# Kernel optimization log

Hardware: AMD Instinct MI355X
Metric: run time of the kernel (lower is better)

The kernel has to match this reference:

```python
import jax, jax.numpy as jnp
import numpy as np

P = 120000   # total pillars across batch
C = 64       # num_input_features
B = 4
NX = 512
NY = 512


def setup_inputs() -> dict:
    key = jax.random.key(0)
    k1, k2, k3, k4 = jax.random.split(key, 4)
    voxel_features = jax.random.normal(k1, (P, C), dtype=jnp.float32)
    b = jax.random.randint(k2, (P, 1), 0, B, dtype=jnp.int32)
    z = jnp.zeros((P, 1), dtype=jnp.int32)
    y = jax.random.randint(k3, (P, 1), 0, NY, dtype=jnp.int32)
    x = jax.random.randint(k4, (P, 1), 0, NX, dtype=jnp.int32)
    coords = jnp.concatenate([b, z, y, x], axis=1)  # [P, 4] = (batch, z, y, x)
    return {"voxel_features": voxel_features, "coords": coords,
            "batch_size": B, "nx": NX, "ny": NY}


def reference(voxel_features, coords, batch_size, nx, ny):
    # Fused scatter: flat index = batch*ny*nx + y*nx + x (single pass, no per-batch loop).
    flat = (coords[:, 0].astype(jnp.int32) * (ny * nx)
            + coords[:, 2].astype(jnp.int32) * nx
            + coords[:, 3].astype(jnp.int32))  # [P]
    canvas = jnp.zeros((batch_size * ny * nx, voxel_features.shape[1]),
                       dtype=voxel_features.dtype)
    canvas = canvas.at[flat].set(voxel_features)          # [B*ny*nx, C]
    canvas = canvas.reshape(batch_size, ny, nx, -1)       # [B, ny, nx, C]
    return canvas.transpose(0, 3, 1, 2)                   # [B, C, ny, nx]
```

## Files before the change

kernel.cpp:

```cpp
#include <hip/hip_runtime.h>
#include <hip/hip_bf16.h>


#define NXC 512
#define NYC 512
#define BC 4
#define CC 64
#define SLOTS_PER_BATCH (NXC * NYC)
#define TOTAL_SLOTS (BC * SLOTS_PER_BATCH)

typedef float vf4 __attribute__((ext_vector_type(4)));

__global__ void build_winner_kernel(const int* __restrict__ coords,
                                    int* __restrict__ winner, int P) {
    int p = blockIdx.x * blockDim.x + threadIdx.x;
    if (p >= P) return;
    int4 c = ((const int4*)coords)[p];
    int flat = c.x * SLOTS_PER_BATCH + c.z * NXC + c.w;
    atomicMax(&winner[flat], p);
}

__global__ __launch_bounds__(256) void scatter_out_kernel(
        const float* __restrict__ vf,
        const int* __restrict__ winner,
        float* __restrict__ out) {
    int blk = blockIdx.x;
    int h   = blk & 1;
    int tq  = ((blk >> 1) << 8) + threadIdx.x;
    int b   = tq >> 16;
    int rem = (tq << 2) & (SLOTS_PER_BATCH - 1);

    int4 w = ((const int4*)winner)[tq];

    float* obase = out + (size_t)b * (CC * SLOTS_PER_BATCH)
                       + (size_t)(h << 5) * SLOTS_PER_BATCH + rem;
    const int coff = h << 3;
    const vf4* v0 = (const vf4*)(vf + (size_t)w.x * CC) + coff;
    const vf4* v1 = (const vf4*)(vf + (size_t)w.y * CC) + coff;
    const vf4* v2 = (const vf4*)(vf + (size_t)w.z * CC) + coff;
    const vf4* v3 = (const vf4*)(vf + (size_t)w.w * CC) + coff;

    const vf4 z4 = (vf4)(0.f);
    #pragma unroll
    for (int j = 0; j < 8; ++j) {
        vf4 a = z4, bb = z4, cc = z4, dd = z4;
        if (w.x >= 0) a  = v0[j];
        if (w.y >= 0) bb = v1[j];
        if (w.z >= 0) cc = v2[j];
        if (w.w >= 0) dd = v3[j];

        vf4* s0 = (vf4*)(obase + (size_t)(4 * j + 0) * SLOTS_PER_BATCH);
        vf4* s1 = (vf4*)(obase + (size_t)(4 * j + 1) * SLOTS_PER_BATCH);
        vf4* s2 = (vf4*)(obase + (size_t)(4 * j + 2) * SLOTS_PER_BATCH);
        vf4* s3 = (vf4*)(obase + (size_t)(4 * j + 3) * SLOTS_PER_BATCH);
        vf4 r0 = {a.x, bb.x, cc.x, dd.x};
        vf4 r1 = {a.y, bb.y, cc.y, dd.y};
        vf4 r2 = {a.z, bb.z, cc.z, dd.z};
        vf4 r3 = {a.w, bb.w, cc.w, dd.w};
        __builtin_nontemporal_store(r0, s0);
        __builtin_nontemporal_store(r1, s1);
        __builtin_nontemporal_store(r2, s2);
        __builtin_nontemporal_store(r3, s3);
    }
}

extern "C" void kernel_launch(void* const* d_in, const int* in_sizes, int n_in,
                              void* d_out, int out_size, void* d_ws, size_t ws_size,
                              hipStream_t stream) {
    const float* vf    = (const float*)d_in[0];
    const int* coords  = (const int*)d_in[1];
    int P = in_sizes[0] / CC;

    int* winner = (int*)d_ws;
    float* out  = (float*)d_out;

    (void)hipMemsetAsync(winner, 0xFF, (size_t)TOTAL_SLOTS * sizeof(int), stream);

    build_winner_kernel<<<(P + 255) / 256, 256, 0, stream>>>(coords, winner, P);

    scatter_out_kernel<<<(TOTAL_SLOTS / 4 / 256) * 2, 256, 0, stream>>>(vf, winner, out);
}
```

Measured before the change: 299.3 us.

## Remap scatter blocks to chunk-by-channel-quad grid with XCD-aware chunk placement

```diff
diff --git a/kernel.cpp b/kernel.cpp
--- a/kernel.cpp
+++ b/kernel.cpp
@@ -8,6 +8,9 @@
 #define CC 64
 #define SLOTS_PER_BATCH (NXC * NYC)
 #define TOTAL_SLOTS (BC * SLOTS_PER_BATCH)
+#define CHUNK_SLOTS 8192
+#define NCHUNK (TOTAL_SLOTS / CHUNK_SLOTS)
+#define NCQ (CC / 4)
 
 typedef float vf4 __attribute__((ext_vector_type(4)));
 
@@ -24,43 +27,41 @@
         const float* __restrict__ vf,
         const int* __restrict__ winner,
         float* __restrict__ out) {
-    int blk = blockIdx.x;
-    int h   = blk & 1;
-    int tq  = ((blk >> 1) << 8) + threadIdx.x;
-    int b   = tq >> 16;
-    int rem = (tq << 2) & (SLOTS_PER_BATCH - 1);
+    int raw = blockIdx.x;
+    int xcd = raw & 7;
+    int i   = raw >> 3;
+    int cq    = i & 15;
+    int chunk = ((i >> 4) << 3) | xcd;
 
-    int4 w = ((const int4*)winner)[tq];
+    int t     = threadIdx.x;
+    int qbase = chunk * (CHUNK_SLOTS / 4);
+    int slot0 = chunk * CHUNK_SLOTS;
+    int b     = slot0 >> 18;
+    int rem0  = slot0 & (SLOTS_PER_BATCH - 1);
 
-    float* obase = out + (size_t)b * (CC * SLOTS_PER_BATCH)
-                       + (size_t)(h << 5) * SLOTS_PER_BATCH + rem;
-    const int coff = h << 3;
-    const vf4* v0 = (const vf4*)(vf + (size_t)w.x * CC) + coff;
-    const vf4* v1 = (const vf4*)(vf + (size_t)w.y * CC) + coff;
-    const vf4* v2 = (const vf4*)(vf + (size_t)w.z * CC) + coff;
-    const vf4* v3 = (const vf4*)(vf + (size_t)w.w * CC) + coff;
+    float* obase = out + ((size_t)b * CC + (size_t)(cq << 2)) * SLOTS_PER_BATCH;
 
     const vf4 z4 = (vf4)(0.f);
     #pragma unroll
-    for (int j = 0; j < 8; ++j) {
+    for (int g = 0; g < 8; ++g) {
+        int q = (g << 8) + t;
+        int4 w = ((const int4*)winner)[qbase + q];
+        int rem = rem0 + (q << 2);
+
         vf4 a = z4, bb = z4, cc = z4, dd = z4;
-        if (w.x >= 0) a  = v0[j];
-        if (w.y >= 0) bb = v1[j];
-        if (w.z >= 0) cc = v2[j];
-        if (w.w >= 0) dd = v3[j];
+        if (w.x >= 0) a  = ((const vf4*)(vf + (size_t)w.x * CC))[cq];
+        if (w.y >= 0) bb = ((const vf4*)(vf + (size_t)w.y * CC))[cq];
+        if (w.z >= 0) cc = ((const vf4*)(vf + (size_t)w.z * CC))[cq];
+        if (w.w >= 0) dd = ((const vf4*)(vf + (size_t)w.w * CC))[cq];
 
-        vf4* s0 = (vf4*)(obase + (size_t)(4 * j + 0) * SLOTS_PER_BATCH);
-        vf4* s1 = (vf4*)(obase + (size_t)(4 * j + 1) * SLOTS_PER_BATCH);
-        vf4* s2 = (vf4*)(obase + (size_t)(4 * j + 2) * SLOTS_PER_BATCH);
-        vf4* s3 = (vf4*)(obase + (size_t)(4 * j + 3) * SLOTS_PER_BATCH);
         vf4 r0 = {a.x, bb.x, cc.x, dd.x};
         vf4 r1 = {a.y, bb.y, cc.y, dd.y};
         vf4 r2 = {a.z, bb.z, cc.z, dd.z};
         vf4 r3 = {a.w, bb.w, cc.w, dd.w};
-        __builtin_nontemporal_store(r0, s0);
-        __builtin_nontemporal_store(r1, s1);
-        __builtin_nontemporal_store(r2, s2);
-        __builtin_nontemporal_store(r3, s3);
+        __builtin_nontemporal_store(r0, (vf4*)(obase + (size_t)0 * SLOTS_PER_BATCH + rem));
+        __builtin_nontemporal_store(r1, (vf4*)(obase + (size_t)1 * SLOTS_PER_BATCH + rem));
+        __builtin_nontemporal_store(r2, (vf4*)(obase + (size_t)2 * SLOTS_PER_BATCH + rem));
+        __builtin_nontemporal_store(r3, (vf4*)(obase + (size_t)3 * SLOTS_PER_BATCH + rem));
     }
 }
 
@@ -78,5 +79,5 @@
 
     build_winner_kernel<<<(P + 255) / 256, 256, 0, stream>>>(coords, winner, P);
 
-    scatter_out_kernel<<<(TOTAL_SLOTS / 4 / 256) * 2, 256, 0, stream>>>(vf, winner, out);
+    scatter_out_kernel<<<NCHUNK * NCQ, 256, 0, stream>>>(vf, winner, out);
 }
```

Result: slower. 333.0 us (+11.3%).
